# Performance work log

Hardware: AMD Instinct MI355X
Metric: run time of the kernel (lower is better)

## Reference

```python
import jax, jax.numpy as jnp
import numpy as np

EMBED_DIM = 768
NUM_HEADS = 12
HEAD_DIM = EMBED_DIM // NUM_HEADS
KERNEL = 7


def _neighbor_index(size, kernel):
    # NATTEN border-clamped neighborhood: window start = clip(i - k//2, 0, size-k)
    start = np.clip(np.arange(size) - kernel // 2, 0, size - kernel)
    return jnp.asarray(start[:, None] + np.arange(kernel)[None, :])  # [size, kernel]


def setup_inputs() -> dict:
    key = jax.random.key(0)
    k1, k2, k3, k4, k5 = jax.random.split(key, 5)
    B, H, W, C = 8, 64, 64, EMBED_DIM
    x = jax.random.normal(k1, (B, H, W, C), dtype=jnp.float32)
    # torch.nn.Linear layout: weight [out, in]
    w_qkv = jax.random.normal(k2, (3 * C, C), dtype=jnp.float32) * (C ** -0.5)
    b_qkv = jax.random.normal(k3, (3 * C,), dtype=jnp.float32) * 0.02
    w_proj = jax.random.normal(k4, (C, C), dtype=jnp.float32) * (C ** -0.5)
    b_proj = jax.random.normal(k5, (C,), dtype=jnp.float32) * 0.02
    return {"x": x, "w_qkv": w_qkv, "b_qkv": b_qkv, "w_proj": w_proj, "b_proj": b_proj}


def reference(x, w_qkv, b_qkv, w_proj, b_proj):
    B, H, W, C = x.shape
    scale = HEAD_DIM ** -0.5
    qkv = (x @ w_qkv.T + b_qkv).reshape(B, H, W, 3, NUM_HEADS, HEAD_DIM)
    q = qkv[..., 0, :, :] * scale          # [B,H,W,nh,hd]
    k = qkv[..., 1, :, :]
    v = qkv[..., 2, :, :]

    idx_i = _neighbor_index(H, KERNEL)      # [H,K]
    idx_j = _neighbor_index(W, KERNEL)      # [W,K]

    # Logits over the K*K local neighborhood, one shifted gather per offset
    # (avoids materializing [B,H,W,K2,nh,hd]).
    logits = []
    for ki in range(KERNEL):
        k_row = jnp.take(k, idx_i[:, ki], axis=1)          # [B,H,W,nh,hd]
        for kj in range(KERNEL):
            k_nb = jnp.take(k_row, idx_j[:, kj], axis=2)   # [B,H,W,nh,hd]
            logits.append(jnp.einsum('bhwnd,bhwnd->bhwn', q, k_nb))
    logits = jnp.stack(logits, axis=-1)                     # [B,H,W,nh,K2]
    attn = jax.nn.softmax(logits, axis=-1)

    out = jnp.zeros((B, H, W, NUM_HEADS, HEAD_DIM), dtype=x.dtype)
    off = 0
    for ki in range(KERNEL):
        v_row = jnp.take(v, idx_i[:, ki], axis=1)
        for kj in range(KERNEL):
            v_nb = jnp.take(v_row, idx_j[:, kj], axis=2)
            out = out + attn[..., off][..., None] * v_nb
            off += 1

    out = out.reshape(B, H, W, C)
    return out @ w_proj.T + b_proj
```

## Files before the change

kernel.cpp:

```cpp
#include <hip/hip_runtime.h>
#include <cstddef>

#define EMBED   768
#define NHEADS  12
#define HDIM    64
#define KSZ     7
#define IMG_H   64
#define IMG_W   64
#define BATCH   8
#define NTOK    (BATCH*IMG_H*IMG_W)
#define QKV_N   (3*EMBED)

typedef __attribute__((ext_vector_type(8))) short  bf16x8;
typedef __attribute__((ext_vector_type(4))) float  f32x4;
typedef __attribute__((ext_vector_type(8))) unsigned short u16x8;
typedef __attribute__((ext_vector_type(4))) unsigned short u16x4;

__device__ __forceinline__ unsigned short f2bf(float f) {
    unsigned int u = __float_as_uint(f);
    u += 0x7FFFu + ((u >> 16) & 1u);
    return (unsigned short)(u >> 16);
}

__device__ __forceinline__ void gload_lds16(const void* g, void* l) {
    __builtin_amdgcn_global_load_lds(
        (const __attribute__((address_space(1))) unsigned int*)g,
        (__attribute__((address_space(3))) unsigned int*)l, 16, 0, 0);
}

__global__ __launch_bounds__(256)
void cvt_bf16_kernel(const float* __restrict__ in, unsigned short* __restrict__ out, int n4)
{
    int i = blockIdx.x * 256 + threadIdx.x;
    if (i < n4) {
        float4 f = *(const float4*)(in + (size_t)i * 4);
        u16x4 o;
        o[0] = f2bf(f.x); o[1] = f2bf(f.y); o[2] = f2bf(f.z); o[3] = f2bf(f.w);
        *(u16x4*)(out + (size_t)i * 4) = o;
    }
}

template<int BF16OUT>
__global__ __launch_bounds__(512)
void gemm256(const unsigned short* __restrict__ A, const unsigned short* __restrict__ W,
             const float* __restrict__ bias, void* __restrict__ outp,
             int M, int N, int K, int scaleN, float scale)
{
    __shared__ unsigned short lds[3 * 16384];
    const int t_ = threadIdx.x;
    const int l = t_ & 63, w = t_ >> 6;
    const int wr2 = w >> 2, wc4 = w & 3;

    const int nbx = M >> 8;
    const int lin = blockIdx.x;
    const int cpx = gridDim.x >> 3;
    const int swz = (lin & 7) * cpx + (lin >> 3);
    const int bm = (swz % nbx) << 8;
    const int bn = (swz / nbx) << 8;

    const int kperm = ((l & 3) ^ ((l >> 3) & 3)) * 8;
    const unsigned short* gA = A + (size_t)(bm + w * 16 + (l >> 2)) * K + kperm;
    const unsigned short* gB = W + (size_t)(bn + w * 16 + (l >> 2)) * K + kperm;
    const size_t step8 = (size_t)128 * K;

    unsigned short* lA = lds + w * 512;
    unsigned short* lB = lds + 8192 + w * 512;

    const int foff = (l & 15) * 32 + (((l >> 4) ^ ((l >> 1) & 3)) * 8);
    const unsigned short* raw = lds + (wr2 * 8) * 512 + foff;
    const unsigned short* rbw = lds + 8192 + (wc4 * 4) * 512 + foff;

    f32x4 acc[8][4] = {};
    const int NT = K / 32;

    gload_lds16(gA, lA);              gload_lds16(gA + step8, lA + 4096);
    gload_lds16(gB, lB);              gload_lds16(gB + step8, lB + 4096);
    gload_lds16(gA + 32, lA + 16384); gload_lds16(gA + step8 + 32, lA + 16384 + 4096);
    gload_lds16(gB + 32, lB + 16384); gload_lds16(gB + step8 + 32, lB + 16384 + 4096);
    asm volatile("s_waitcnt vmcnt(4)" ::: "memory");
    __builtin_amdgcn_s_barrier();

    for (int t = 0; t < NT; ++t) {
        const int q  = (t % 3) * 16384;
        const int qn = ((t + 2) % 3) * 16384;
        const bool pf = (t + 2 < NT);
        const int ko = t * 32 + 64;

        if (pf) { gload_lds16(gA + ko, lA + qn); gload_lds16(gA + step8 + ko, lA + qn + 4096); }
        bf16x8 af0[4], bf[4];
        #pragma unroll
        for (int m = 0; m < 4; ++m) af0[m] = *(const bf16x8*)(raw + q + m * 512);
        #pragma unroll
        for (int n = 0; n < 4; ++n) bf[n]  = *(const bf16x8*)(rbw + q + n * 512);
        __builtin_amdgcn_s_barrier();
        __builtin_amdgcn_s_setprio(1);
        #pragma unroll
        for (int m = 0; m < 4; ++m)
            #pragma unroll
            for (int n = 0; n < 4; ++n)
                acc[m][n] = __builtin_amdgcn_mfma_f32_16x16x32_bf16(af0[m], bf[n], acc[m][n], 0, 0, 0);
        __builtin_amdgcn_s_setprio(0);
        __builtin_amdgcn_s_barrier();

        if (pf) { gload_lds16(gB + ko, lB + qn); gload_lds16(gB + step8 + ko, lB + qn + 4096); }
        bf16x8 af1[4];
        #pragma unroll
        for (int m = 0; m < 4; ++m) af1[m] = *(const bf16x8*)(raw + q + (4 + m) * 512);
        __builtin_amdgcn_s_barrier();
        __builtin_amdgcn_s_setprio(1);
        #pragma unroll
        for (int m = 0; m < 4; ++m)
            #pragma unroll
            for (int n = 0; n < 4; ++n)
                acc[4 + m][n] = __builtin_amdgcn_mfma_f32_16x16x32_bf16(af1[m], bf[n], acc[4 + m][n], 0, 0, 0);
        __builtin_amdgcn_s_setprio(0);
        if (t < NT - 1) {
            if (pf) asm volatile("s_waitcnt vmcnt(4)" ::: "memory");
            else    asm volatile("s_waitcnt vmcnt(0)" ::: "memory");
            __builtin_amdgcn_s_barrier();
        }
    }

    const int cr = (l >> 4) * 4;
    const int cc = l & 15;
    #pragma unroll
    for (int m = 0; m < 8; ++m) {
        #pragma unroll
        for (int n = 0; n < 4; ++n) {
            const int col = bn + wc4 * 64 + n * 16 + cc;
            const float bv = bias[col];
            const bool sc = col < scaleN;
            #pragma unroll
            for (int r = 0; r < 4; ++r) {
                const int row = bm + wr2 * 128 + m * 16 + cr + r;
                float v = acc[m][n][r] + bv;
                if (sc) v *= scale;
                if (BF16OUT) ((unsigned short*)outp)[(size_t)row * N + col] = f2bf(v);
                else         ((float*)outp)[(size_t)row * N + col] = v;
            }
        }
    }
}

__global__ __launch_bounds__(256)
void natten_kernel(const unsigned short* __restrict__ qkv, unsigned short* __restrict__ attn_bf)
{
    __shared__ unsigned short smem[4 * 5888];
    const int t = threadIdx.x;
    const int w = t >> 6, l = t & 63;
    const int c15 = l & 15, g = l >> 4;
    const int blk = blockIdx.x;
    const int tg = blk & 15;
    const int h = (blk >> 4) % NHEADS;
    const int b = blk / (16 * NHEADS);
    const int ti = (tg >> 2) * 16, tj = (tg & 3) * 16;
    const int pi0 = ti + w * 4;
    const int ws = min(max(pi0 - 3, 0), IMG_H - 10);
    const int cs = min(max(tj - 3, 0), IMG_W - 22);
    const int pixbase = b * 4096;

    unsigned short* Kl = smem + w * 5888;
    unsigned short* Vt = Kl + 2304;

    const int pj = tj + c15;
    const int sj = min(max(pj - 3, 0), IMG_W - KSZ);
    const unsigned int cm = 0x7Fu << (sj - cs);
    unsigned int rm[4];
    #pragma unroll
    for (int qt = 0; qt < 4; ++qt) {
        int si = min(max(pi0 + qt - 3, 0), IMG_H - KSZ);
        rm[qt] = 0x7Fu << (si - ws);
    }

    bf16x8 qf[4][2];
    #pragma unroll
    for (int qt = 0; qt < 4; ++qt)
        #pragma unroll
        for (int dh = 0; dh < 2; ++dh)
            qf[qt][dh] = *(const bf16x8*)(qkv +
                (size_t)(pixbase + (pi0 + qt) * 64 + tj + c15) * QKV_N + h * HDIM + dh * 32 + g * 8);

    const int sr = l & 31;
    const int h5 = l >> 5;
    const int sig = ((sr & 12) << 1) | ((sr & 16) >> 2) | (sr & 3);

    u16x8 kst[4], vst[4];

    {
        int ur = sr / 22, uc = sr - ur * 22;
        int prow = min(ws + ur, IMG_H - 1);
        const u16x8* gk = (const u16x8*)(qkv +
            (size_t)(pixbase + prow * 64 + cs + uc) * QKV_N + EMBED + h * HDIM + h5 * 32);
        #pragma unroll
        for (int i = 0; i < 4; ++i) { kst[i] = gk[i]; vst[i] = gk[i + 96]; }
    }
    #pragma unroll
    for (int i = 0; i < 4; ++i) *(u16x8*)(Kl + sr * 72 + h5 * 32 + i * 8) = kst[i];
    #pragma unroll
    for (int i = 0; i < 4; ++i)
        #pragma unroll
        for (int e = 0; e < 8; ++e)
            Vt[(h5 * 32 + i * 8 + e) * 56 + sig] = vst[i][e];

    f32x4 oacc[4][4] = {};
    float spart[4] = {0.f, 0.f, 0.f, 0.f};

    #pragma unroll 1
    for (int C = 0; C < 7; ++C) {
        if (C < 6) {
            int kk = (C + 1) * 32 + sr;
            int ur = kk / 22, uc = kk - ur * 22;
            int prow = min(ws + ur, IMG_H - 1);
            const u16x8* gk = (const u16x8*)(qkv +
                (size_t)(pixbase + prow * 64 + cs + uc) * QKV_N + EMBED + h * HDIM + h5 * 32);
            #pragma unroll
            for (int i = 0; i < 4; ++i) { kst[i] = gk[i]; vst[i] = gk[i + 96]; }
        }

        bf16x8 ka[2][2], vb[4];
        #pragma unroll
        for (int kt = 0; kt < 2; ++kt)
            #pragma unroll
            for (int dh = 0; dh < 2; ++dh)
                ka[kt][dh] = *(const bf16x8*)(Kl + (kt * 16 + c15) * 72 + dh * 32 + g * 8);
        #pragma unroll
        for (int dt = 0; dt < 4; ++dt)
            vb[dt] = *(const bf16x8*)(Vt + (dt * 16 + c15) * 56 + g * 8);

        int kk0 = C * 32 + 4 * g;
        int a22 = kk0 / 22;
        int uc0 = kk0 - a22 * 22;
        int urx[2][4]; unsigned int cb[2][4];
        #pragma unroll
        for (int kt = 0; kt < 2; ++kt)
            #pragma unroll
            for (int r = 0; r < 4; ++r) {
                int x = uc0 + kt * 16 + r;
                int wrp = x >= 22;
                int uc = x - (wrp ? 22 : 0);
                urx[kt][r] = a22 + wrp;
                cb[kt][r] = (cm >> uc) & 1u;
            }

        #pragma unroll
        for (int qt = 0; qt < 4; ++qt) {
            f32x4 s0 = {}, s1 = {};
            s0 = __builtin_amdgcn_mfma_f32_16x16x32_bf16(ka[0][0], qf[qt][0], s0, 0, 0, 0);
            s0 = __builtin_amdgcn_mfma_f32_16x16x32_bf16(ka[0][1], qf[qt][1], s0, 0, 0, 0);
            s1 = __builtin_amdgcn_mfma_f32_16x16x32_bf16(ka[1][0], qf[qt][0], s1, 0, 0, 0);
            s1 = __builtin_amdgcn_mfma_f32_16x16x32_bf16(ka[1][1], qf[qt][1], s1, 0, 0, 0);
            float p[2][4];
            #pragma unroll
            for (int r = 0; r < 4; ++r) {
                float e0 = exp2f(s0[r]);
                float e1 = exp2f(s1[r]);
                p[0][r] = ((rm[qt] >> urx[0][r]) & cb[0][r]) ? e0 : 0.f;
                p[1][r] = ((rm[qt] >> urx[1][r]) & cb[1][r]) ? e1 : 0.f;
                spart[qt] += p[0][r] + p[1][r];
            }
            unsigned int pk[4];
            asm("v_cvt_pk_bf16_f32 %0, %1, %2" : "=v"(pk[0]) : "v"(p[0][0]), "v"(p[0][1]));
            asm("v_cvt_pk_bf16_f32 %0, %1, %2" : "=v"(pk[1]) : "v"(p[0][2]), "v"(p[0][3]));
            asm("v_cvt_pk_bf16_f32 %0, %1, %2" : "=v"(pk[2]) : "v"(p[1][0]), "v"(p[1][1]));
            asm("v_cvt_pk_bf16_f32 %0, %1, %2" : "=v"(pk[3]) : "v"(p[1][2]), "v"(p[1][3]));
            bf16x8 pa = *(bf16x8*)pk;
            #pragma unroll
            for (int dt = 0; dt < 4; ++dt)
                oacc[qt][dt] = __builtin_amdgcn_mfma_f32_16x16x32_bf16(pa, vb[dt], oacc[qt][dt], 0, 0, 0);
        }

        if (C < 6) {
            #pragma unroll
            for (int i = 0; i < 4; ++i) *(u16x8*)(Kl + sr * 72 + h5 * 32 + i * 8) = kst[i];
            #pragma unroll
            for (int i = 0; i < 4; ++i)
                #pragma unroll
                for (int e = 0; e < 8; ++e)
                    Vt[(h5 * 32 + i * 8 + e) * 56 + sig] = vst[i][e];
        }
    }

    #pragma unroll
    for (int qt = 0; qt < 4; ++qt) {
        float s = spart[qt];
        s += __shfl_xor(s, 16);
        s += __shfl_xor(s, 32);
        #pragma unroll
        for (int r = 0; r < 4; ++r) {
            float sb = __shfl(s, 4 * g + r);
            float inv = __builtin_amdgcn_rcpf(sb);
            size_t obase = (size_t)(pixbase + (pi0 + qt) * 64 + tj + 4 * g + r) * EMBED
                         + h * HDIM + c15;
            #pragma unroll
            for (int dt = 0; dt < 4; ++dt)
                attn_bf[obase + dt * 16] = f2bf(oacc[qt][dt][r] * inv);
        }
    }
}

extern "C" void kernel_launch(void* const* d_in, const int* in_sizes, int n_in,
                              void* d_out, int out_size, void* d_ws, size_t ws_size,
                              hipStream_t stream)
{
    const float* x      = (const float*)d_in[0];
    const float* w_qkv  = (const float*)d_in[1];
    const float* b_qkv  = (const float*)d_in[2];
    const float* w_proj = (const float*)d_in[3];
    const float* b_proj = (const float*)d_in[4];
    float* out = (float*)d_out;

    char* p = (char*)d_ws;
    unsigned short* qkv = (unsigned short*)p;     p += (size_t)NTOK * QKV_N * 2;
    unsigned short* xbf = (unsigned short*)p;
    unsigned short* attn_bf = xbf;                p += (size_t)NTOK * EMBED * 2;
    unsigned short* wq_bf = (unsigned short*)p;   p += (size_t)QKV_N * EMBED * 2;
    unsigned short* wp_bf = (unsigned short*)p;

    const float scale = 0.125f * 1.44269504088896f;

    {
        int n4 = NTOK * EMBED / 4;
        cvt_bf16_kernel<<<(n4 + 255) / 256, 256, 0, stream>>>(x, xbf, n4);
        n4 = QKV_N * EMBED / 4;
        cvt_bf16_kernel<<<(n4 + 255) / 256, 256, 0, stream>>>(w_qkv, wq_bf, n4);
        n4 = EMBED * EMBED / 4;
        cvt_bf16_kernel<<<(n4 + 255) / 256, 256, 0, stream>>>(w_proj, wp_bf, n4);
    }

    {
        gemm256<1><<<(NTOK / 256) * (QKV_N / 256), 512, 0, stream>>>(
            xbf, wq_bf, b_qkv, qkv, NTOK, QKV_N, EMBED, EMBED, scale);
    }

    natten_kernel<<<BATCH * NHEADS * 16, 256, 0, stream>>>(qkv, attn_bf);

    {
        gemm256<0><<<(NTOK / 256) * (EMBED / 256), 512, 0, stream>>>(
            attn_bf, wp_bf, b_proj, out, NTOK, EMBED, EMBED, 0, 1.0f);
    }
}
```

Baseline: 337.5 us.

## Stage GEMM epilogue through LDS for vector stores and remap blocks per XCD

The GEMM epilogue now writes each wave's 16-row accumulator slice into a swizzled LDS buffer, then reads it back so each lane writes contiguous 16-byte vectors to global memory. This replaces scattered 2- and 4-byte stores. Block-to-tile mapping is also changed so each XCD owns a contiguous band of M rows and walks all N tiles, which aims to improve L2 reuse of A. The m loop is marked unroll 1 while indexing the acc register array by m. That may force the accumulators into scratch memory.

```diff
diff --git a/kernel.cpp b/kernel.cpp
--- a/kernel.cpp
+++ b/kernel.cpp
@@ -51,12 +51,11 @@
     const int l = t_ & 63, w = t_ >> 6;
     const int wr2 = w >> 2, wc4 = w & 3;
 
-    const int nbx = M >> 8;
-    const int lin = blockIdx.x;
-    const int cpx = gridDim.x >> 3;
-    const int swz = (lin & 7) * cpx + (lin >> 3);
-    const int bm = (swz % nbx) << 8;
-    const int bn = (swz / nbx) << 8;
+    const int nby = N >> 8;
+    const int xcd = blockIdx.x & 7;
+    const int loc = blockIdx.x >> 3;
+    const int bm = (xcd * ((M >> 8) >> 3) + loc / nby) << 8;
+    const int bn = (loc % nby) << 8;
 
     const int kperm = ((l & 3) ^ ((l >> 3) & 3)) * 8;
     const unsigned short* gA = A + (size_t)(bm + w * 16 + (l >> 2)) * K + kperm;
@@ -121,22 +120,57 @@
         }
     }
 
+    __syncthreads();
     const int cr = (l >> 4) * 4;
     const int cc = l & 15;
-    #pragma unroll
-    for (int m = 0; m < 8; ++m) {
-        #pragma unroll
-        for (int n = 0; n < 4; ++n) {
-            const int col = bn + wc4 * 64 + n * 16 + cc;
-            const float bv = bias[col];
-            const bool sc = col < scaleN;
-            #pragma unroll
-            for (int r = 0; r < 4; ++r) {
-                const int row = bm + wr2 * 128 + m * 16 + cr + r;
-                float v = acc[m][n][r] + bv;
-                if (sc) v *= scale;
-                if (BF16OUT) ((unsigned short*)outp)[(size_t)row * N + col] = f2bf(v);
-                else         ((float*)outp)[(size_t)row * N + col] = v;
+    const int g  = l >> 4;
+    const int erd = l >> 2;
+    const int ecs = l & 3;
+
+    if (BF16OUT) {
+        unsigned short* eb = lds + w * 1024;
+        unsigned short* out16 = (unsigned short*)outp;
+        #pragma unroll 1
+        for (int m = 0; m < 8; ++m) {
+            #pragma unroll
+            for (int n = 0; n < 4; ++n) {
+                const int col = bn + wc4 * 64 + n * 16 + cc;
+                const float bv = bias[col];
+                const bool sc = col < scaleN;
+                #pragma unroll
+                for (int r = 0; r < 4; ++r) {
+                    float v = acc[m][n][r] + bv;
+                    if (sc) v *= scale;
+                    eb[(cr + r) * 64 + ((n * 16 + cc) ^ (g << 4))] = f2bf(v);
+                }
+            }
+            const int rowg = bm + wr2 * 128 + m * 16 + erd;
+            const unsigned short* rp = eb + erd * 64 + ((ecs ^ (erd >> 2)) << 4);
+            u16x8 v0 = *(const u16x8*)rp;
+            u16x8 v1 = *(const u16x8*)(rp + 8);
+            unsigned short* gp = out16 + (size_t)rowg * N + bn + wc4 * 64 + ecs * 16;
+            *(u16x8*)gp = v0;
+            *(u16x8*)(gp + 8) = v1;
+        }
+    } else {
+        float* eb = (float*)(void*)lds + w * 1024;
+        float* outf = (float*)outp;
+        #pragma unroll 1
+        for (int m = 0; m < 8; ++m) {
+            #pragma unroll
+            for (int n = 0; n < 4; ++n) {
+                const int col = bn + wc4 * 64 + n * 16 + cc;
+                const float bv = bias[col];
+                #pragma unroll
+                for (int r = 0; r < 4; ++r)
+                    eb[(cr + r) * 64 + ((n * 16 + cc) ^ (g << 3))] = acc[m][n][r] + bv;
+            }
+            const int rowg = bm + wr2 * 128 + m * 16 + erd;
+            float* gp = outf + (size_t)rowg * N + bn + wc4 * 64 + ecs * 16;
+            #pragma unroll
+            for (int qq = 0; qq < 4; ++qq) {
+                f32x4 vv = *(const f32x4*)(eb + erd * 64 + (((ecs * 16 + qq * 4) ^ ((erd >> 2) << 3))));
+                *(f32x4*)(gp + qq * 4) = vv;
             }
         }
     }
```

Result: slower. 526.1 us (+55.9%).

## Restructure GEMM mainloop to double-buffered BK=64 tiles with interleaved prefetch

Applied to the files above, without the earlier changes.

The bf16 MFMA GEMM moves from a triple-buffered K=32 pipeline to a double-buffered K=64 stage, using 128KB of LDS. Each loop iteration now runs four MFMA sub-phases, with global-to-LDS loads for the next stage issued between them. This halves the number of loop iterations and amortizes barriers and waits over more math. The cost is larger LDS use, which may limit occupancy, and only a single stage of prefetch lookahead.

```diff
diff --git a/kernel.cpp b/kernel.cpp
--- a/kernel.cpp
+++ b/kernel.cpp
@@ -46,80 +46,110 @@
              const float* __restrict__ bias, void* __restrict__ outp,
              int M, int N, int K, int scaleN, float scale)
 {
-    __shared__ unsigned short lds[3 * 16384];
+    __shared__ unsigned short lds[65536];
     const int t_ = threadIdx.x;
     const int l = t_ & 63, w = t_ >> 6;
-    const int wr2 = w >> 2, wc4 = w & 3;
+    const int wm = w >> 2, wn = w & 3;
 
     const int nbx = M >> 8;
+    const int cpx = gridDim.x >> 3;
     const int lin = blockIdx.x;
-    const int cpx = gridDim.x >> 3;
     const int swz = (lin & 7) * cpx + (lin >> 3);
     const int bm = (swz % nbx) << 8;
     const int bn = (swz / nbx) << 8;
 
-    const int kperm = ((l & 3) ^ ((l >> 3) & 3)) * 8;
-    const unsigned short* gA = A + (size_t)(bm + w * 16 + (l >> 2)) * K + kperm;
-    const unsigned short* gB = W + (size_t)(bn + w * 16 + (l >> 2)) * K + kperm;
-    const size_t step8 = (size_t)128 * K;
-
-    unsigned short* lA = lds + w * 512;
-    unsigned short* lB = lds + 8192 + w * 512;
-
+    const int kperm8 = ((l & 3) ^ ((l >> 3) & 3)) * 8;
+    const unsigned short* gA = A + (size_t)(bm + 2 * w * 16 + (l >> 2)) * K + kperm8;
+    const unsigned short* gB = W + (size_t)(bn + 2 * w * 16 + (l >> 2)) * K + kperm8;
+    const size_t rstep = (size_t)16 * K;
+
+    const int dA = w * 2048;
     const int foff = (l & 15) * 32 + (((l >> 4) ^ ((l >> 1) & 3)) * 8);
-    const unsigned short* raw = lds + (wr2 * 8) * 512 + foff;
-    const unsigned short* rbw = lds + 8192 + (wc4 * 4) * 512 + foff;
+    const int aoff = wm * 8192;
+    const int boff = 16384 + wn * 4096;
 
     f32x4 acc[8][4] = {};
-    const int NT = K / 32;
-
-    gload_lds16(gA, lA);              gload_lds16(gA + step8, lA + 4096);
-    gload_lds16(gB, lB);              gload_lds16(gB + step8, lB + 4096);
-    gload_lds16(gA + 32, lA + 16384); gload_lds16(gA + step8 + 32, lA + 16384 + 4096);
-    gload_lds16(gB + 32, lB + 16384); gload_lds16(gB + step8 + 32, lB + 16384 + 4096);
-    asm volatile("s_waitcnt vmcnt(4)" ::: "memory");
-    __builtin_amdgcn_s_barrier();
+    const int NT = K / 64;
+
+#define BARRIER() asm volatile("s_barrier" ::: "memory")
+#define WAITV4()  asm volatile("s_waitcnt vmcnt(4)" ::: "memory")
+#define WAITV0()  asm volatile("s_waitcnt vmcnt(0)" ::: "memory")
+#define STGA(c, k0, kk) do { \
+        gload_lds16(gA + (size_t)(k0) + (kk) * 32,         lds + (c) + dA + (kk) * 512); \
+        gload_lds16(gA + rstep + (size_t)(k0) + (kk) * 32, lds + (c) + dA + (2 + (kk)) * 512); } while (0)
+#define STGB(c, k0, kk) do { \
+        gload_lds16(gB + (size_t)(k0) + (kk) * 32,         lds + (c) + 16384 + dA + (kk) * 512); \
+        gload_lds16(gB + rstep + (size_t)(k0) + (kk) * 32, lds + (c) + 16384 + dA + (2 + (kk)) * 512); } while (0)
+
+    STGA(0, 0, 0); STGB(0, 0, 0); STGA(0, 0, 1); STGB(0, 0, 1);
+    WAITV4();
+    BARRIER();
 
     for (int t = 0; t < NT; ++t) {
-        const int q  = (t % 3) * 16384;
-        const int qn = ((t + 2) % 3) * 16384;
-        const bool pf = (t + 2 < NT);
-        const int ko = t * 32 + 64;
-
-        if (pf) { gload_lds16(gA + ko, lA + qn); gload_lds16(gA + step8 + ko, lA + qn + 4096); }
-        bf16x8 af0[4], bf[4];
-        #pragma unroll
-        for (int m = 0; m < 4; ++m) af0[m] = *(const bf16x8*)(raw + q + m * 512);
-        #pragma unroll
-        for (int n = 0; n < 4; ++n) bf[n]  = *(const bf16x8*)(rbw + q + n * 512);
-        __builtin_amdgcn_s_barrier();
+        const int c  = (t & 1) << 15;
+        const int cn = c ^ 32768;
+        const int k1 = (t + 1) * 64;
+        const bool pf = (t + 1) < NT;
+
+        bf16x8 a[4], bq[4];
+
+        #pragma unroll
+        for (int m = 0; m < 4; ++m) a[m]  = *(const bf16x8*)(lds + c + aoff + (m * 2) * 512 + foff);
+        #pragma unroll
+        for (int n = 0; n < 4; ++n) bq[n] = *(const bf16x8*)(lds + c + boff + (n * 2) * 512 + foff);
+        if (pf) STGA(cn, k1, 0);
+        BARRIER();
         __builtin_amdgcn_s_setprio(1);
         #pragma unroll
         for (int m = 0; m < 4; ++m)
             #pragma unroll
             for (int n = 0; n < 4; ++n)
-                acc[m][n] = __builtin_amdgcn_mfma_f32_16x16x32_bf16(af0[m], bf[n], acc[m][n], 0, 0, 0);
+                acc[m][n] = __builtin_amdgcn_mfma_f32_16x16x32_bf16(a[m], bq[n], acc[m][n], 0, 0, 0);
         __builtin_amdgcn_s_setprio(0);
-        __builtin_amdgcn_s_barrier();
-
-        if (pf) { gload_lds16(gB + ko, lB + qn); gload_lds16(gB + step8 + ko, lB + qn + 4096); }
-        bf16x8 af1[4];
-        #pragma unroll
-        for (int m = 0; m < 4; ++m) af1[m] = *(const bf16x8*)(raw + q + (4 + m) * 512);
-        __builtin_amdgcn_s_barrier();
+
+        #pragma unroll
+        for (int m = 0; m < 4; ++m) a[m] = *(const bf16x8*)(lds + c + aoff + ((4 + m) * 2) * 512 + foff);
+        if (pf) { STGB(cn, k1, 0); WAITV4(); } else { WAITV0(); }
+        BARRIER();
         __builtin_amdgcn_s_setprio(1);
         #pragma unroll
         for (int m = 0; m < 4; ++m)
             #pragma unroll
             for (int n = 0; n < 4; ++n)
-                acc[4 + m][n] = __builtin_amdgcn_mfma_f32_16x16x32_bf16(af1[m], bf[n], acc[4 + m][n], 0, 0, 0);
+                acc[4 + m][n] = __builtin_amdgcn_mfma_f32_16x16x32_bf16(a[m], bq[n], acc[4 + m][n], 0, 0, 0);
         __builtin_amdgcn_s_setprio(0);
-        if (t < NT - 1) {
-            if (pf) asm volatile("s_waitcnt vmcnt(4)" ::: "memory");
-            else    asm volatile("s_waitcnt vmcnt(0)" ::: "memory");
-            __builtin_amdgcn_s_barrier();
-        }
-    }
+
+        #pragma unroll
+        for (int m = 0; m < 4; ++m) a[m]  = *(const bf16x8*)(lds + c + aoff + (m * 2 + 1) * 512 + foff);
+        #pragma unroll
+        for (int n = 0; n < 4; ++n) bq[n] = *(const bf16x8*)(lds + c + boff + (n * 2 + 1) * 512 + foff);
+        if (pf) STGA(cn, k1, 1);
+        BARRIER();
+        __builtin_amdgcn_s_setprio(1);
+        #pragma unroll
+        for (int m = 0; m < 4; ++m)
+            #pragma unroll
+            for (int n = 0; n < 4; ++n)
+                acc[m][n] = __builtin_amdgcn_mfma_f32_16x16x32_bf16(a[m], bq[n], acc[m][n], 0, 0, 0);
+        __builtin_amdgcn_s_setprio(0);
+
+        #pragma unroll
+        for (int m = 0; m < 4; ++m) a[m] = *(const bf16x8*)(lds + c + aoff + ((4 + m) * 2 + 1) * 512 + foff);
+        if (pf) { STGB(cn, k1, 1); WAITV4(); }
+        BARRIER();
+        __builtin_amdgcn_s_setprio(1);
+        #pragma unroll
+        for (int m = 0; m < 4; ++m)
+            #pragma unroll
+            for (int n = 0; n < 4; ++n)
+                acc[4 + m][n] = __builtin_amdgcn_mfma_f32_16x16x32_bf16(a[m], bq[n], acc[4 + m][n], 0, 0, 0);
+        __builtin_amdgcn_s_setprio(0);
+    }
+#undef BARRIER
+#undef WAITV4
+#undef WAITV0
+#undef STGA
+#undef STGB
 
     const int cr = (l >> 4) * 4;
     const int cc = l & 15;
@@ -127,12 +157,12 @@
     for (int m = 0; m < 8; ++m) {
         #pragma unroll
         for (int n = 0; n < 4; ++n) {
-            const int col = bn + wc4 * 64 + n * 16 + cc;
+            const int col = bn + wn * 64 + n * 16 + cc;
             const float bv = bias[col];
             const bool sc = col < scaleN;
             #pragma unroll
             for (int r = 0; r < 4; ++r) {
-                const int row = bm + wr2 * 128 + m * 16 + cr + r;
+                const int row = bm + wm * 128 + m * 16 + cr + r;
                 float v = acc[m][n][r] + bv;
                 if (sc) v *= scale;
                 if (BF16OUT) ((unsigned short*)outp)[(size_t)row * N + col] = f2bf(v);
```

After: 325.9 us. -3.4%, faster.
